# Kernel optimization log

Hardware: AMD Instinct MI355X
Metric: run time of the kernel (lower is better)

The kernel has to match this reference:

```python
import itertools
import jax, jax.numpy as jnp
import numpy as np

MESH_SIZE = np.array([8, 8, 8, 8], dtype=np.int32)   # lattice granularity per dim
VOLUME = int(np.prod(MESH_SIZE))                      # 4096
BATCH = 32768
NDIM = len(MESH_SIZE)


def setup_inputs() -> dict:
    key = jax.random.key(0)
    k1, k2 = jax.random.split(key)
    coordinates = jax.random.uniform(k1, (BATCH, NDIM), dtype=jnp.float32)  # in [0,1]
    mesh_pred = jax.random.normal(k2, (BATCH, VOLUME), dtype=jnp.float32)
    return {"coordinates": coordinates, "mesh_pred": mesh_pred}


def reference(coordinates, mesh_pred):
    mesh = jnp.asarray(MESH_SIZE)                       # [d]
    # row-major strides: coef[i] = prod(mesh[i+1:])
    coef = jnp.asarray(np.concatenate([np.cumprod(MESH_SIZE[::-1])[::-1][1:], [1]]).astype(np.int32))
    # get_index: scale to lattice, truncate (coords >= 0 so trunc == floor), clamp to [0, s-2]
    c = coordinates * (mesh - 1).astype(coordinates.dtype)          # [B, d]
    ci = jnp.clip(c.astype(jnp.int32), 0, mesh - 2)                 # [B, d] int
    frac = c - ci.astype(c.dtype)                                   # [B, d]
    # all 2^d corner offsets
    corners = jnp.asarray(list(itertools.product([0, 1], repeat=NDIM)), dtype=jnp.int32)  # [2^d, d]
    # flat lattice index for each corner: [B, 2^d]
    idx = jnp.sum((ci[:, None, :] + corners[None, :, :]) * coef, axis=-1)
    vals = jnp.take_along_axis(mesh_pred, idx, axis=1)              # [B, 2^d]
    # weight per corner: prod_d (1-frac) if offset 0 else frac, via 1-d-frac*(1-2d)
    cf = corners.astype(c.dtype)
    w = jnp.prod(1.0 - cf - frac[:, None, :] * (1.0 - 2.0 * cf), axis=-1)  # [B, 2^d]
    return jnp.sum(vals * w, axis=1)                                # [B]
```

## Files before the change

kernel.cpp:

```cpp
#include <hip/hip_runtime.h>

#define BATCH   32768
#define VOLUME  4096
#define NBLK    (BATCH / 64)

__global__ __launch_bounds__(64) void interp4d_kernel(
    const float* __restrict__ coords,
    const float* __restrict__ mesh,
    float* __restrict__ out)
{
    const int b = blockIdx.x * 64 + threadIdx.x;
    if (b >= BATCH) return;

    const float4 c4 = *reinterpret_cast<const float4*>(coords + (size_t)b * 4);

    const float c0 = c4.x * 7.0f;
    const float c1 = c4.y * 7.0f;
    const float c2 = c4.z * 7.0f;
    const float c3 = c4.w * 7.0f;

    int i0 = (int)c0; i0 = i0 < 0 ? 0 : (i0 > 6 ? 6 : i0);
    int i1 = (int)c1; i1 = i1 < 0 ? 0 : (i1 > 6 ? 6 : i1);
    int i2 = (int)c2; i2 = i2 < 0 ? 0 : (i2 > 6 ? 6 : i2);
    int i3 = (int)c3; i3 = i3 < 0 ? 0 : (i3 > 6 ? 6 : i3);

    const float f0 = c0 - (float)i0;
    const float f1 = c1 - (float)i1;
    const float f2 = c2 - (float)i2;
    const float f3 = c3 - (float)i3;

    const float* __restrict__ base =
        mesh + (size_t)b * VOLUME + i0 * 512 + i1 * 64 + i2 * 8 + i3;

    float v[16];
#pragma unroll
    for (int a = 0; a < 2; ++a)
#pragma unroll
        for (int bb = 0; bb < 2; ++bb)
#pragma unroll
            for (int cc = 0; cc < 2; ++cc)
#pragma unroll
                for (int d = 0; d < 2; ++d)
                    v[a * 8 + bb * 4 + cc * 2 + d] =
                        base[a * 512 + bb * 64 + cc * 8 + d];

    const float w0[2] = {1.0f - f0, f0};
    const float w1[2] = {1.0f - f1, f1};
    const float w2[2] = {1.0f - f2, f2};
    const float w3[2] = {1.0f - f3, f3};

    float acc = 0.0f;
#pragma unroll
    for (int a = 0; a < 2; ++a)
#pragma unroll
        for (int bb = 0; bb < 2; ++bb)
#pragma unroll
            for (int cc = 0; cc < 2; ++cc)
#pragma unroll
                for (int d = 0; d < 2; ++d)
                    acc += v[a * 8 + bb * 4 + cc * 2 + d] *
                           (w0[a] * w1[bb] * w2[cc] * w3[d]);

    out[b] = acc;
}

extern "C" void kernel_launch(void* const* d_in, const int* in_sizes, int n_in,
                              void* d_out, int out_size, void* d_ws, size_t ws_size,
                              hipStream_t stream) {
    const float* coords = (const float*)d_in[0];
    const float* mesh   = (const float*)d_in[1];
    float* out          = (float*)d_out;

    interp4d_kernel<<<NBLK, 64, 0, stream>>>(coords, mesh, out);
}
```

Baseline: 568.9 us.

## Split each sample's 16 corner gathers across 8 threads with shuffle reduction

Each batch row is now handled by 8 lanes instead of one thread. Each lane gathers one pair of adjacent corners (two floats), weights them, and a 3-step xor-shuffle reduction combines the partials. This raises the thread count and the number of outstanding memory requests, so the latency-bound scattered gathers run with far more parallelism, and the block size goes to 256. In exchange, the coordinate load is repeated across the 8 lanes and shuffle overhead is added.

After: 567.4 us. No clear change (-0.3%).

```diff
diff --git a/kernel.cpp b/kernel.cpp
--- a/kernel.cpp
+++ b/kernel.cpp
@@ -2,17 +2,21 @@
 
 #define BATCH   32768
 #define VOLUME  4096
-#define NBLK    (BATCH / 64)
+#define TPR     8
+#define NTHREADS (BATCH * TPR)
+#define BLOCK   256
+#define NBLK    (NTHREADS / BLOCK)
 
-__global__ __launch_bounds__(64) void interp4d_kernel(
+__global__ __launch_bounds__(BLOCK) void interp4d_kernel(
     const float* __restrict__ coords,
     const float* __restrict__ mesh,
     float* __restrict__ out)
 {
-    const int b = blockIdx.x * 64 + threadIdx.x;
-    if (b >= BATCH) return;
+    const int t = blockIdx.x * BLOCK + threadIdx.x;
+    const int r = t >> 3;
+    const int k = t & 7;
 
-    const float4 c4 = *reinterpret_cast<const float4*>(coords + (size_t)b * 4);
+    const float4 c4 = *reinterpret_cast<const float4*>(coords + (size_t)r * 4);
 
     const float c0 = c4.x * 7.0f;
     const float c1 = c4.y * 7.0f;
@@ -29,39 +33,27 @@
     const float f2 = c2 - (float)i2;
     const float f3 = c3 - (float)i3;
 
-    const float* __restrict__ base =
-        mesh + (size_t)b * VOLUME + i0 * 512 + i1 * 64 + i2 * 8 + i3;
+    const int a  = (k >> 2) & 1;
+    const int bb = (k >> 1) & 1;
+    const int cc = k & 1;
 
-    float v[16];
-#pragma unroll
-    for (int a = 0; a < 2; ++a)
-#pragma unroll
-        for (int bb = 0; bb < 2; ++bb)
-#pragma unroll
-            for (int cc = 0; cc < 2; ++cc)
-#pragma unroll
-                for (int d = 0; d < 2; ++d)
-                    v[a * 8 + bb * 4 + cc * 2 + d] =
-                        base[a * 512 + bb * 64 + cc * 8 + d];
+    const float* __restrict__ p =
+        mesh + (size_t)r * VOLUME + (i0 + a) * 512 + (i1 + bb) * 64 + (i2 + cc) * 8 + i3;
 
-    const float w0[2] = {1.0f - f0, f0};
-    const float w1[2] = {1.0f - f1, f1};
-    const float w2[2] = {1.0f - f2, f2};
-    const float w3[2] = {1.0f - f3, f3};
+    const float v0 = p[0];
+    const float v1 = p[1];
 
-    float acc = 0.0f;
-#pragma unroll
-    for (int a = 0; a < 2; ++a)
-#pragma unroll
-        for (int bb = 0; bb < 2; ++bb)
-#pragma unroll
-            for (int cc = 0; cc < 2; ++cc)
-#pragma unroll
-                for (int d = 0; d < 2; ++d)
-                    acc += v[a * 8 + bb * 4 + cc * 2 + d] *
-                           (w0[a] * w1[bb] * w2[cc] * w3[d]);
+    const float w = (a  ? f0 : 1.0f - f0) *
+                    (bb ? f1 : 1.0f - f1) *
+                    (cc ? f2 : 1.0f - f2);
 
-    out[b] = acc;
+    float partial = w * (v0 * (1.0f - f3) + v1 * f3);
+
+    partial += __shfl_xor(partial, 1);
+    partial += __shfl_xor(partial, 2);
+    partial += __shfl_xor(partial, 4);
+
+    if (k == 0) out[r] = partial;
 }
 
 extern "C" void kernel_launch(void* const* d_in, const int* in_sizes, int n_in,
@@ -71,5 +63,5 @@
     const float* mesh   = (const float*)d_in[1];
     float* out          = (float*)d_out;
 
-    interp4d_kernel<<<NBLK, 64, 0, stream>>>(coords, mesh, out);
+    interp4d_kernel<<<NBLK, BLOCK, 0, stream>>>(coords, mesh, out);
 }
```
